# Optimization experiments

Measured on AMD Instinct MI355X. Metric: run time of the kernel, lower is better.

Reference implementation:

```python
import jax, jax.numpy as jnp
from jax import lax
import numpy as np

NUM_HEAD = 4
D_MODEL = 160
HEAD_DIM = D_MODEL // NUM_HEAD  # 40
FEAT_DIM = 64
F_SIZE = (128, 128)
B = 4
LN_EPS = 1e-5
LEAKY_SLOPE = 0.01
DN = ('NCHW', 'OIHW', 'NCHW')


def setup_inputs() -> dict:
    key = jax.random.key(0)
    ks = jax.random.split(key, 10)
    pe_len = (F_SIZE[0] // 2) * (F_SIZE[1] // 2) + 1  # 4097
    s = 0.05
    return {
        'x': jax.random.normal(ks[0], (B, FEAT_DIM, F_SIZE[0], F_SIZE[1]), jnp.float32),
        'conv1_w': jax.random.normal(ks[1], (FEAT_DIM, FEAT_DIM, 2, 2), jnp.float32) * s,
        'conv1_b': jax.random.normal(ks[2], (FEAT_DIM,), jnp.float32) * s,
        'conv2_w': jax.random.normal(ks[3], (D_MODEL, FEAT_DIM, 1, 1), jnp.float32) * s,
        'conv2_b': jax.random.normal(ks[4], (D_MODEL,), jnp.float32) * s,
        'pe': jax.random.uniform(ks[5], (pe_len, 1), jnp.float32),
        'wq': jax.random.normal(ks[6], (D_MODEL, D_MODEL), jnp.float32) * s,
        'wk': jax.random.normal(ks[7], (D_MODEL, D_MODEL), jnp.float32) * s,
        'wv': jax.random.normal(ks[8], (D_MODEL, D_MODEL), jnp.float32) * s,
        'ln_w': jnp.ones((D_MODEL,), jnp.float32),
        'ln_b': jnp.zeros((D_MODEL,), jnp.float32),
    }


def reference(x, conv1_w, conv1_b, conv2_w, conv2_b, pe, wq, wk, wv, ln_w, ln_b):
    b = x.shape[0]
    # patch embed: stride-2 conv -> 1x1 conv -> LeakyReLU
    f = lax.conv_general_dilated(x, conv1_w, (2, 2), 'VALID', dimension_numbers=DN)
    f = f + conv1_b[None, :, None, None]
    f = lax.conv_general_dilated(f, conv2_w, (1, 1), 'VALID', dimension_numbers=DN)
    f = f + conv2_b[None, :, None, None]
    f = jnp.where(f >= 0, f, LEAKY_SLOPE * f)
    _, c, h, w = f.shape  # [b, 160, 64, 64]
    f = f.reshape(b, c, h * w).transpose(0, 2, 1)  # [b, s, d]
    # pad one extra token at end of sequence, add positional encoding [s+1, 1]
    f = jnp.pad(f, ((0, 0), (0, 1), (0, 0))) + pe  # [b, s+1, d]
    s1 = f.shape[1]
    # torch Linear (no bias): y = x @ W.T
    q = (f @ wq.T).reshape(b, s1, NUM_HEAD, HEAD_DIM).transpose(0, 2, 1, 3)
    k = (f @ wk.T).reshape(b, s1, NUM_HEAD, HEAD_DIM).transpose(0, 2, 1, 3)
    v = (f @ wv.T).reshape(b, s1, NUM_HEAD, HEAD_DIM).transpose(0, 2, 1, 3)
    score = jnp.einsum('bhqd,bhkd->bhqk', q, k) / jnp.sqrt(jnp.float32(HEAD_DIM))
    score = jax.nn.softmax(score, axis=-1)
    att = jnp.einsum('bhqk,bhkd->bhqd', score, v)  # [b, h, s+1, hd]
    cat = att.transpose(0, 2, 1, 3).reshape(b, s1, D_MODEL)
    feat = cat[:, :-1, :]  # drop padded token -> [b, s, d]
    # residual LayerNorm: LN(feat) + feat
    mu = jnp.mean(feat, axis=-1, keepdims=True)
    var = jnp.mean(jnp.square(feat - mu), axis=-1, keepdims=True)
    ln = (feat - mu) / jnp.sqrt(var + LN_EPS) * ln_w + ln_b
    feat = ln + feat
    feat = feat.transpose(0, 2, 1).reshape(b, D_MODEL, h, w)  # [b, 160, 64, 64]
    feat = jnp.repeat(jnp.repeat(feat, 2, axis=2), 2, axis=3)
    return feat
```

## Files before the change

kernel.cpp:

```cpp
#include <hip/hip_runtime.h>

typedef _Float16 f16;
typedef _Float16 half2v __attribute__((ext_vector_type(2)));
typedef _Float16 half4v __attribute__((ext_vector_type(4)));
typedef _Float16 half8 __attribute__((ext_vector_type(8)));
typedef float f32x4 __attribute__((ext_vector_type(4)));
typedef unsigned u32x4 __attribute__((ext_vector_type(4)));

#define MFMA16(a, b, c) __builtin_amdgcn_mfma_f32_16x16x32_f16((a), (b), (c), 0, 0, 0)

__device__ __forceinline__ unsigned pk2(float a, float b) {
  return __builtin_bit_cast(unsigned, __builtin_amdgcn_cvt_pkrtz(a, b));
}

__device__ __forceinline__ void plswap_pair(unsigned& a, unsigned& b) {
  asm("s_nop 1\n\t"
      "v_permlane32_swap_b32 %0, %1\n\t"
      "v_permlane16_swap_b32 %0, %1"
      : "+v"(a), "+v"(b));
}


__global__ __launch_bounds__(256) void k_convqkv(
    const float* __restrict__ x, const float* __restrict__ w1, const float* __restrict__ b1,
    const float* __restrict__ w2, const float* __restrict__ b2, const float* __restrict__ pe,
    const float* __restrict__ wq, const float* __restrict__ wk, const float* __restrict__ wv,
    f16* __restrict__ q_h, f16* __restrict__ k_h, f16* __restrict__ vt_h,
    float* __restrict__ kmaxp) {
  __shared__ __attribute__((aligned(16))) char smem[112192];
  f16* fT   = (f16*)smem;
  f16* xh   = (f16*)(smem + 21504);
  f16* wT   = (f16*)(smem + 21504);
  float* red = (float*)(smem + 48384);
  f16* w1h  = (f16*)(smem + 55360);
  f16* c1t  = (f16*)(smem + 55360);
  float* red160 = (float*)(smem + 64576);
  f16* w2h  = (f16*)(smem + 89152);

  int y = blockIdx.x, b = blockIdx.y;
  int t = threadIdx.x, lane = t & 63, wv4 = t >> 6, quad = lane >> 4, col = lane & 15;
  int s0 = y * 64;

  const float* xb = x + (b * 64) * 16384 + (2 * y) * 128;
#pragma unroll
  for (int it = 0; it < 32; ++it) {
    int flat = t + it * 256;
    int pos = flat & 63, r = (flat >> 6) & 1, ci = flat >> 7;
    float2 v = *(const float2*)(xb + ci * 16384 + r * 128 + 2 * pos);
    *(unsigned*)(xh + pos * 264 + ci * 4 + r * 2) = pk2(v.x, v.y);
  }
#pragma unroll
  for (int it = 0; it < 16; ++it) {
    int i4 = t + it * 256;
    int co = i4 >> 6, q4 = (i4 & 63) * 4;
    f32x4 v = *(const f32x4*)(w1 + co * 256 + q4);
    uint2 u = {pk2(v[0], v[1]), pk2(v[2], v[3])};
    *(uint2*)(w1h + co * 264 + q4) = u;
  }
#pragma unroll
  for (int it = 0; it < 10; ++it) {
    int i4 = t + it * 256;
    int c2 = i4 >> 4, q4 = (i4 & 15) * 4;
    f32x4 v = *(const f32x4*)(w2 + c2 * 160 / 160 * 0 + c2 * 64 + q4);
    uint2 u = {pk2(v[0], v[1]), pk2(v[2], v[3])};
    *(uint2*)(w2h + c2 * 72 + q4) = u;
  }
  __syncthreads();

  float b1v[4];
#pragma unroll
  for (int r = 0; r < 4; ++r) b1v[r] = b1[wv4 * 16 + quad * 4 + r];
  f32x4 acc1[4];
#pragma unroll
  for (int nt = 0; nt < 4; ++nt)
#pragma unroll
    for (int r = 0; r < 4; ++r) acc1[nt][r] = b1v[r];
#pragma unroll
  for (int kk = 0; kk < 8; ++kk) {
    half8 a = *(half8*)(w1h + (wv4 * 16 + col) * 264 + kk * 32 + quad * 8);
#pragma unroll
    for (int nt = 0; nt < 4; ++nt) {
      half8 bfr = *(half8*)(xh + (nt * 16 + col) * 264 + kk * 32 + quad * 8);
      acc1[nt] = MFMA16(a, bfr, acc1[nt]);
    }
  }
  __syncthreads();
#pragma unroll
  for (int nt = 0; nt < 4; ++nt) {
    uint2 u = {pk2(acc1[nt][0], acc1[nt][1]), pk2(acc1[nt][2], acc1[nt][3])};
    *(uint2*)(c1t + (nt * 16 + col) * 72 + wv4 * 16 + quad * 4) = u;
  }
  __syncthreads();

  f32x4 acc2[10];
#pragma unroll
  for (int mt = 0; mt < 10; ++mt)
#pragma unroll
    for (int r = 0; r < 4; ++r) acc2[mt][r] = b2[mt * 16 + quad * 4 + r];
  half8 bb0 = *(half8*)(c1t + (wv4 * 16 + col) * 72 + quad * 8);
  half8 bb1 = *(half8*)(c1t + (wv4 * 16 + col) * 72 + 32 + quad * 8);
#pragma unroll
  for (int mt = 0; mt < 10; ++mt) {
    half8 a0 = *(half8*)(w2h + (mt * 16 + col) * 72 + quad * 8);
    half8 a1 = *(half8*)(w2h + (mt * 16 + col) * 72 + 32 + quad * 8);
    acc2[mt] = MFMA16(a0, bb0, acc2[mt]);
    acc2[mt] = MFMA16(a1, bb1, acc2[mt]);
  }
  float pes = pe[s0 + wv4 * 16 + col];
#pragma unroll
  for (int mt = 0; mt < 10; ++mt) {
    float p[4];
#pragma unroll
    for (int r = 0; r < 4; ++r) {
      float v = acc2[mt][r];
      v = (v >= 0.f) ? v : 0.01f * v;
      p[r] = v + pes;
    }
    uint2 u = {pk2(p[0], p[1]), pk2(p[2], p[3])};
    *(uint2*)(fT + (wv4 * 16 + col) * 168 + mt * 16 + quad * 4) = u;
  }
  __syncthreads();

  half8 af[5];
  int rowA = wv4 * 16 + col;
#pragma unroll
  for (int kk = 0; kk < 5; ++kk)
    af[kk] = *(half8*)(fT + rowA * 168 + kk * 32 + quad * 8);

  float ks0[4], ks1[4];
#pragma unroll
  for (int r = 0; r < 4; ++r) { ks0[r] = 0.f; ks1[r] = 0.f; }

  for (int kind = 0; kind < 3; ++kind) {
    const float* wsp = (kind == 0) ? wq : (kind == 1 ? wk : wv);
    for (int hf = 0; hf < 2; ++hf) {
      __syncthreads();
      for (int c = t; c < 1600; c += 256) {
        int row = c / 20, seg = c - row * 20;
        const float* src = wsp + (hf * 80 + row) * 160 + seg * 8;
        f32x4 va = *(const f32x4*)src;
        f32x4 vb = *(const f32x4*)(src + 4);
        uint4 u = {pk2(va[0], va[1]), pk2(va[2], va[3]), pk2(vb[0], vb[1]), pk2(vb[2], vb[3])};
        *(uint4*)(wT + row * 168 + seg * 8) = u;
      }
      __syncthreads();
#pragma unroll
      for (int n0 = 0; n0 < 5; ++n0) {
        f32x4 acc; acc[0] = 0.f; acc[1] = 0.f; acc[2] = 0.f; acc[3] = 0.f;
        int rowB = n0 * 16 + col;
#pragma unroll
        for (int kk = 0; kk < 5; ++kk) {
          half8 bf = *(half8*)(wT + rowB * 168 + kk * 32 + quad * 8);
          acc = MFMA16(af[kk], bf, acc);
        }
        int o = (hf * 5 + n0) * 16 + col;
        int hh = o / 40, d = o - hh * 40;
        int bh = b * 4 + hh;
        if (kind == 1) {
          bool kidx = (n0 * 16 + col) >= 40;
#pragma unroll
          for (int r = 0; r < 4; ++r) {
            float z = acc[r] * acc[r];
            ks0[r] += kidx ? 0.f : z;
            ks1[r] += kidx ? z : 0.f;
          }
        }
#pragma unroll
        for (int r = 0; r < 4; ++r) {
          int s = s0 + wv4 * 16 + quad * 4 + r;
          f16 v = (f16)acc[r];
          if (kind == 0)      q_h[((size_t)bh * 4097 + s) * 40 + d] = v;
          else if (kind == 1) k_h[((size_t)bh * 4160 + s) * 40 + d] = v;
          else                vt_h[((size_t)bh * 40 + d) * 4160 + s] = v;
        }
      }
      if (kind == 1) {
        float m0 = 0.f, m1 = 0.f;
#pragma unroll
        for (int r = 0; r < 4; ++r) {
          float v0 = ks0[r], v1 = ks1[r];
          v0 += __shfl_xor(v0, 1); v0 += __shfl_xor(v0, 2);
          v0 += __shfl_xor(v0, 4); v0 += __shfl_xor(v0, 8);
          v1 += __shfl_xor(v1, 1); v1 += __shfl_xor(v1, 2);
          v1 += __shfl_xor(v1, 4); v1 += __shfl_xor(v1, 8);
          m0 = fmaxf(m0, v0); m1 = fmaxf(m1, v1);
          ks0[r] = 0.f; ks1[r] = 0.f;
        }
        m0 = fmaxf(m0, __shfl_xor(m0, 16)); m0 = fmaxf(m0, __shfl_xor(m0, 32));
        m1 = fmaxf(m1, __shfl_xor(m1, 16)); m1 = fmaxf(m1, __shfl_xor(m1, 32));
        if (lane == 0) { red[wv4 * 4 + hf * 2] = m0; red[wv4 * 4 + hf * 2 + 1] = m1; }
      }
    }
  }
  __syncthreads();
  if (t < 4) {
    float m = fmaxf(fmaxf(red[t], red[4 + t]), fmaxf(red[8 + t], red[12 + t]));
    kmaxp[(b * 4 + t) * 65 + y] = m;
  }

  if (y == 63) {
    float pe4 = pe[4096];
    if (t < 160) {
      int hh = t / 40, d = t - hh * 40, bh = b * 4 + hh;
#pragma unroll
      for (int kind = 0; kind < 3; ++kind) {
        const float* wsp = (kind == 0) ? wq : (kind == 1 ? wk : wv);
        const float* wr = wsp + t * 160;
        float rs = 0.f;
#pragma unroll
        for (int c4 = 0; c4 < 40; ++c4) {
          f32x4 v = *(const f32x4*)(wr + c4 * 4);
          rs += v[0] + v[1] + v[2] + v[3];
        }
        float val = pe4 * rs;
        if (kind == 0)      q_h[((size_t)bh * 4097 + 4096) * 40 + d] = (f16)val;
        else if (kind == 1) { k_h[((size_t)bh * 4160 + 4096) * 40 + d] = (f16)val;
                              red160[t] = val * val; }
        else                vt_h[((size_t)bh * 40 + d) * 4160 + 4096] = (f16)val;
      }
    }
    __syncthreads();
    if (t < 4) {
      float s = 0.f;
#pragma unroll
      for (int j = 0; j < 40; ++j) s += red160[t * 40 + j];
      kmaxp[(b * 4 + t) * 65 + 64] = s;
    }
  }
}

__global__ __launch_bounds__(256, 4) void k_attn(
    const f16* __restrict__ q_h, const f16* __restrict__ k_h,
    const f16* __restrict__ vt_h, const float* __restrict__ kmaxp,
    float* __restrict__ pacc) {
  __shared__ __attribute__((aligned(16))) f16 Ks[2][64 * 40];
  __shared__ __attribute__((aligned(16))) f16 Vs[2][40 * 72];
  __shared__ __attribute__((aligned(16))) f16 Ones[8];
  __shared__ __attribute__((aligned(16))) f16 Zro[8];
  __shared__ __attribute__((aligned(16))) float red4[4];

  int qt = blockIdx.x, bh = blockIdx.y, ks = blockIdx.z;
  int qbase = qt * 128;
  int t = threadIdx.x, lane = t & 63, wv = t >> 6, quad = lane >> 4, col = lane & 15;
  const float c1l = 0.15811388300841898f * 1.4426950408889634f;
  int gbase = ks * 33;
  int nIter = 33 - ks;

  if (t < 8) { Zro[t] = (f16)0; Ones[t] = (f16)1; }
  {
    float vm = (t < 65) ? kmaxp[bh * 65 + t] : 0.f;
#pragma unroll
    for (int d = 1; d < 64; d <<= 1) vm = fmaxf(vm, __shfl_xor(vm, d));
    if (lane == 0) red4[wv] = vm;
  }

  const f16* khb = k_h + ((size_t)bh * 4160 + gbase * 64) * 40;
  const f16* vtb = vt_h + (size_t)bh * 40 * 4160;
  int vrow = t >> 3, vseg = t & 7;
  uint4 rka = *(const uint4*)(khb + t * 8);
  uint4 rkb = {0, 0, 0, 0}, rvb = {0, 0, 0, 0};
  if (t < 64) rkb = *(const uint4*)(khb + (256 + t) * 8);
  uint4 rva = *(const uint4*)(vtb + vrow * 4160 + gbase * 64 + vseg * 8);
  if (t < 64) rvb = *(const uint4*)(vtb + (32 + vrow) * 4160 + gbase * 64 + vseg * 8);

  half8 zero8;
#pragma unroll
  for (int j = 0; j < 8; ++j) zero8[j] = (f16)0;

  half8 bq[2][2];
#pragma unroll
  for (int nt = 0; nt < 2; ++nt) {
    const f16* qr = q_h + ((size_t)bh * 4097 + qbase + wv * 32 + nt * 16 + col) * 40;
    bq[nt][0] = *(const half8*)(qr + quad * 8);
    bq[nt][1] = (quad == 0) ? *(const half8*)(qr + 32) : zero8;
  }
  __syncthreads();

  float mk = fmaxf(fmaxf(red4[0], red4[1]), fmaxf(red4[2], red4[3]));

  float mfl[2];
#pragma unroll
  for (int nt = 0; nt < 2; ++nt) {
    float s = 0.f;
#pragma unroll
    for (int j = 0; j < 8; ++j) {
      float a0 = (float)bq[nt][0][j], a1 = (float)bq[nt][1][j];
      s += a0 * a0 + a1 * a1;
    }
    s += __shfl_xor(s, 16);
    s += __shfl_xor(s, 32);
    mfl[nt] = sqrtf(s * mk) * c1l - 14.0f;
  }

  f32x4 o_[2][3];
#pragma unroll
  for (int a = 0; a < 2; ++a)
#pragma unroll
    for (int b2 = 0; b2 < 3; ++b2)
#pragma unroll
      for (int r = 0; r < 4; ++r) o_[a][b2][r] = 0.f;

  for (int kt = 0; kt < nIter; ++kt) {
    int bsel = kt & 1;
    int g = gbase + kt;
    *(uint4*)(&Ks[bsel][t * 8]) = rka;
    if (t < 64) *(uint4*)(&Ks[bsel][(256 + t) * 8]) = rkb;
    *(uint4*)(&Vs[bsel][vrow * 72 + vseg * 8]) = rva;
    if (t < 64) *(uint4*)(&Vs[bsel][(32 + vrow) * 72 + vseg * 8]) = rvb;
    if (kt + 1 < nIter) {
      const f16* kn = khb + (size_t)(kt + 1) * 2560;
      int k0n = (g + 1) << 6;
      rka = *(const uint4*)(kn + t * 8);
      if (t < 64) rkb = *(const uint4*)(kn + (256 + t) * 8);
      rva = *(const uint4*)(vtb + vrow * 4160 + k0n + vseg * 8);
      if (t < 64) rvb = *(const uint4*)(vtb + (32 + vrow) * 4160 + k0n + vseg * 8);
    }
    __syncthreads();

    bool lastt = (g == 64);
#pragma unroll
    for (int kk2 = 0; kk2 < 2; ++kk2) {
      f32x4 acc[2][2];
#pragma unroll
      for (int hf = 0; hf < 2; ++hf) {
        int mt = kk2 * 2 + hf;
        int row = mt * 16 + col;
        half8 ak0 = *(half8*)(&Ks[bsel][row * 40 + quad * 8]);
        const f16* pa1 = (quad == 0) ? &Ks[bsel][row * 40 + 32] : Zro;
        half8 ak1 = *(half8*)pa1;
#pragma unroll
        for (int nt = 0; nt < 2; ++nt) {
          f32x4 a; a[0] = 0.f; a[1] = 0.f; a[2] = 0.f; a[3] = 0.f;
          a = MFMA16(ak0, bq[nt][0], a);
          a = MFMA16(ak1, bq[nt][1], a);
          acc[hf][nt] = a;
        }
      }
      half8 pa[2];
#pragma unroll
      for (int nt = 0; nt < 2; ++nt) {
        unsigned sr[4];
#pragma unroll
        for (int hf = 0; hf < 2; ++hf) {
          int mt = kk2 * 2 + hf;
          float p[4];
#pragma unroll
          for (int r = 0; r < 4; ++r) {
            p[r] = __builtin_amdgcn_exp2f(fmaf(acc[hf][nt][r], c1l, -mfl[nt]));
            if (lastt && (mt * 16 + quad * 4 + r) != 0) p[r] = 0.f;
          }
          sr[hf * 2]     = pk2(p[0], p[1]);
          sr[hf * 2 + 1] = pk2(p[2], p[3]);
        }
        plswap_pair(sr[0], sr[2]);
        plswap_pair(sr[1], sr[3]);
        u32x4 uu; uu[0] = sr[0]; uu[1] = sr[1]; uu[2] = sr[2]; uu[3] = sr[3];
        pa[nt] = __builtin_bit_cast(half8, uu);
      }
#pragma unroll
      for (int nv = 0; nv < 3; ++nv) {
        int d = nv * 16 + col;
        const f16* vp = (d < 40) ? &Vs[bsel][d * 72 + kk2 * 32 + quad * 8]
                                 : ((d == 40) ? Ones : Zro);
        half8 bv = *(half8*)vp;
        o_[0][nv] = MFMA16(pa[0], bv, o_[0][nv]);
        o_[1][nv] = MFMA16(pa[1], bv, o_[1][nv]);
      }
    }
  }

  float* pb = pacc + (size_t)(ks * 16 + bh) * 4096 * 48;
#pragma unroll
  for (int mtq = 0; mtq < 2; ++mtq)
#pragma unroll
    for (int nv = 0; nv < 3; ++nv)
#pragma unroll
      for (int r = 0; r < 4; ++r) {
        int q = qbase + wv * 32 + mtq * 16 + quad * 4 + r;
        pb[(size_t)q * 48 + nv * 16 + col] = o_[mtq][nv][r];
      }
}

__global__ __launch_bounds__(256) void k_ln_out(
    const float* __restrict__ pacc, const float* __restrict__ lnw,
    const float* __restrict__ lnb, float* __restrict__ out) {
  __shared__ float g[32 * 164];
  __shared__ float linv[32 * 4];
  int y = blockIdx.x, b = blockIdx.y, z = blockIdx.z, t = threadIdx.x;
  const size_t P1 = (size_t)16 * 4096 * 48;
  int w0 = z * 32;
  if (t < 128) {
    int row = t >> 2, h = t & 3;
    size_t i0 = ((size_t)(b * 4 + h) * 4096 + y * 64 + w0 + row) * 48 + 40;
    linv[row * 4 + h] = 1.f / (pacc[i0] + pacc[P1 + i0]);
  }
  __syncthreads();
#pragma unroll
  for (int it = 0; it < 5; ++it) {
    int flat = t + it * 256;
    int row = flat / 40, dq = flat - row * 40;
    int h = dq / 10, d = (dq - h * 10) * 4;
    size_t idx = ((size_t)(b * 4 + h) * 4096 + y * 64 + w0 + row) * 48 + d;
    f32x4 v0 = *(const f32x4*)(pacc + idx);
    f32x4 v1 = *(const f32x4*)(pacc + P1 + idx);
    float li = linv[row * 4 + h];
    f32x4 gv;
#pragma unroll
    for (int j = 0; j < 4; ++j) gv[j] = (v0[j] + v1[j]) * li;
    *(f32x4*)(g + row * 164 + h * 40 + d) = gv;
  }
  __syncthreads();
  int row = t >> 3, part = t & 7;
  float* gr = g + row * 164 + part * 20;
  float s1 = 0.f, s2 = 0.f;
#pragma unroll
  for (int j4 = 0; j4 < 5; ++j4) {
    f32x4 v = *(f32x4*)(gr + j4 * 4);
#pragma unroll
    for (int j = 0; j < 4; ++j) { s1 += v[j]; s2 += v[j] * v[j]; }
  }
  s1 += __shfl_xor(s1, 1); s1 += __shfl_xor(s1, 2); s1 += __shfl_xor(s1, 4);
  s2 += __shfl_xor(s2, 1); s2 += __shfl_xor(s2, 2); s2 += __shfl_xor(s2, 4);
  float mu = s1 * (1.f / 160.f);
  float var = s2 * (1.f / 160.f) - mu * mu;
  float inv = rsqrtf(var + 1e-5f);
  const float* lw = lnw + part * 20;
  const float* lb = lnb + part * 20;
#pragma unroll
  for (int j = 0; j < 20; ++j) {
    float v = gr[j];
    gr[j] = (v - mu) * inv * lw[j] + lb[j] + v;
  }
  __syncthreads();
  int Yo = t >> 7, xp = t & 63, cpar = (t >> 6) & 1;
  int rl = xp >> 1;
  float* ob = out + (2 * y + Yo) * 128 + z * 64 + xp;
  for (int c = cpar; c < 160; c += 2)
    ob[(size_t)(b * 160 + c) * 16384] = g[rl * 164 + c];
}

extern "C" void kernel_launch(void* const* d_in, const int* in_sizes, int n_in,
                              void* d_out, int out_size, void* d_ws, size_t ws_size,
                              hipStream_t stream) {
  const float* x   = (const float*)d_in[0];
  const float* w1  = (const float*)d_in[1];
  const float* b1  = (const float*)d_in[2];
  const float* w2  = (const float*)d_in[3];
  const float* b2  = (const float*)d_in[4];
  const float* pe  = (const float*)d_in[5];
  const float* wq  = (const float*)d_in[6];
  const float* wk  = (const float*)d_in[7];
  const float* wvp = (const float*)d_in[8];
  const float* lnw = (const float*)d_in[9];
  const float* lnb = (const float*)d_in[10];
  float* out = (float*)d_out;

  char* p = (char*)d_ws;
  f16* q_h   = (f16*)p;   p += (size_t)16 * 4097 * 40 * 2;
  f16* k_h   = (f16*)p;   p += (size_t)16 * 4160 * 40 * 2;
  f16* vt_h  = (f16*)p;   p += (size_t)16 * 40 * 4160 * 2;
  float* pacc = (float*)p; p += (size_t)2 * 16 * 4096 * 48 * 4;
  float* kmaxp = (float*)p; p += 16 * 65 * 4;

  k_convqkv<<<dim3(64, 4), 256, 0, stream>>>(x, w1, b1, w2, b2, pe, wq, wk, wvp,
                                             q_h, k_h, vt_h, kmaxp);
  k_attn<<<dim3(32, 16, 2), 256, 0, stream>>>(q_h, k_h, vt_h, kmaxp, pacc);
  k_ln_out<<<dim3(64, 4, 2), 256, 0, stream>>>(pacc, lnw, lnb, out);
}
```

Baseline: 214.3 us.

## Split attention keys three ways, fold softmax scale and max offset into MFMA

```diff
diff --git a/kernel.cpp b/kernel.cpp
--- a/kernel.cpp
+++ b/kernel.cpp
@@ -34,8 +34,11 @@
   float* red = (float*)(smem + 48384);
   f16* w1h  = (f16*)(smem + 55360);
   f16* c1t  = (f16*)(smem + 55360);
+  f16* Lv   = (f16*)(smem + 55360);
   float* red160 = (float*)(smem + 64576);
   f16* w2h  = (f16*)(smem + 89152);
+
+  const float c1l = 0.15811388300841898f * 1.4426950408889634f;
 
   int y = blockIdx.x, b = blockIdx.y;
   int t = threadIdx.x, lane = t & 63, wv4 = t >> 6, quad = lane >> 4, col = lane & 15;
@@ -61,7 +64,7 @@
   for (int it = 0; it < 10; ++it) {
     int i4 = t + it * 256;
     int c2 = i4 >> 4, q4 = (i4 & 15) * 4;
-    f32x4 v = *(const f32x4*)(w2 + c2 * 160 / 160 * 0 + c2 * 64 + q4);
+    f32x4 v = *(const f32x4*)(w2 + c2 * 64 + q4);
     uint2 u = {pk2(v[0], v[1]), pk2(v[2], v[3])};
     *(uint2*)(w2h + c2 * 72 + q4) = u;
   }
@@ -165,13 +168,18 @@
             ks1[r] += kidx ? z : 0.f;
           }
         }
-#pragma unroll
-        for (int r = 0; r < 4; ++r) {
-          int s = s0 + wv4 * 16 + quad * 4 + r;
-          f16 v = (f16)acc[r];
-          if (kind == 0)      q_h[((size_t)bh * 4097 + s) * 40 + d] = v;
-          else if (kind == 1) k_h[((size_t)bh * 4160 + s) * 40 + d] = v;
-          else                vt_h[((size_t)bh * 40 + d) * 4160 + s] = v;
+        if (kind == 2) {
+          half4v hv;
+#pragma unroll
+          for (int r = 0; r < 4; ++r) hv[r] = (f16)acc[r];
+          *(half4v*)(Lv + (n0 * 16 + col) * 72 + wv4 * 16 + quad * 4) = hv;
+        } else {
+#pragma unroll
+          for (int r = 0; r < 4; ++r) {
+            int s = s0 + wv4 * 16 + quad * 4 + r;
+            if (kind == 0)      q_h[((size_t)bh * 4097 + s) * 40 + d] = (f16)(acc[r] * c1l);
+            else                k_h[((size_t)bh * 4160 + s) * 40 + d] = (f16)acc[r];
+          }
         }
       }
       if (kind == 1) {
@@ -190,6 +198,15 @@
         m1 = fmaxf(m1, __shfl_xor(m1, 16)); m1 = fmaxf(m1, __shfl_xor(m1, 32));
         if (lane == 0) { red[wv4 * 4 + hf * 2] = m0; red[wv4 * 4 + hf * 2 + 1] = m1; }
       }
+      if (kind == 2) {
+        __syncthreads();
+        for (int c = t; c < 640; c += 256) {
+          int row = c >> 3, seg = c & 7;
+          int o = hf * 80 + row, hh = o / 40, d = o - hh * 40;
+          *(uint4*)(vt_h + ((size_t)(b * 4 + hh) * 40 + d) * 4160 + s0 + seg * 8) =
+              *(const uint4*)(Lv + row * 72 + seg * 8);
+        }
+      }
     }
   }
   __syncthreads();
@@ -213,7 +230,7 @@
           rs += v[0] + v[1] + v[2] + v[3];
         }
         float val = pe4 * rs;
-        if (kind == 0)      q_h[((size_t)bh * 4097 + 4096) * 40 + d] = (f16)val;
+        if (kind == 0)      q_h[((size_t)bh * 4097 + 4096) * 40 + d] = (f16)(val * c1l);
         else if (kind == 1) { k_h[((size_t)bh * 4160 + 4096) * 40 + d] = (f16)val;
                               red160[t] = val * val; }
         else                vt_h[((size_t)bh * 40 + d) * 4160 + 4096] = (f16)val;
@@ -229,7 +246,7 @@
   }
 }
 
-__global__ __launch_bounds__(256, 4) void k_attn(
+__global__ __launch_bounds__(256, 6) void k_attn(
     const f16* __restrict__ q_h, const f16* __restrict__ k_h,
     const f16* __restrict__ vt_h, const float* __restrict__ kmaxp,
     float* __restrict__ pacc) {
@@ -242,9 +259,8 @@
   int qt = blockIdx.x, bh = blockIdx.y, ks = blockIdx.z;
   int qbase = qt * 128;
   int t = threadIdx.x, lane = t & 63, wv = t >> 6, quad = lane >> 4, col = lane & 15;
-  const float c1l = 0.15811388300841898f * 1.4426950408889634f;
-  int gbase = ks * 33;
-  int nIter = 33 - ks;
+  int gbase = ks * 22;
+  int nIter = (ks == 2) ? 21 : 22;
 
   if (t < 8) { Zro[t] = (f16)0; Ones[t] = (f16)1; }
   {
@@ -267,29 +283,36 @@
 #pragma unroll
   for (int j = 0; j < 8; ++j) zero8[j] = (f16)0;
 
-  half8 bq[2][2];
+  half8 bq[2][2], q32[2];
 #pragma unroll
   for (int nt = 0; nt < 2; ++nt) {
     const f16* qr = q_h + ((size_t)bh * 4097 + qbase + wv * 32 + nt * 16 + col) * 40;
     bq[nt][0] = *(const half8*)(qr + quad * 8);
-    bq[nt][1] = (quad == 0) ? *(const half8*)(qr + 32) : zero8;
+    q32[nt] = *(const half8*)(qr + 32);
   }
   __syncthreads();
 
   float mk = fmaxf(fmaxf(red4[0], red4[1]), fmaxf(red4[2], red4[3]));
 
-  float mfl[2];
 #pragma unroll
   for (int nt = 0; nt < 2; ++nt) {
     float s = 0.f;
 #pragma unroll
     for (int j = 0; j < 8; ++j) {
-      float a0 = (float)bq[nt][0][j], a1 = (float)bq[nt][1][j];
-      s += a0 * a0 + a1 * a1;
+      float a0 = (float)bq[nt][0][j];
+      s += a0 * a0;
     }
     s += __shfl_xor(s, 16);
     s += __shfl_xor(s, 32);
-    mfl[nt] = sqrtf(s * mk) * c1l - 14.0f;
+#pragma unroll
+    for (int j = 0; j < 8; ++j) {
+      float a1 = (float)q32[nt][j];
+      s += a1 * a1;
+    }
+    float mfl = sqrtf(s * mk) - 14.0f;
+    half8 e = zero8;
+    e[0] = (f16)(-mfl);
+    bq[nt][1] = (quad == 0) ? q32[nt] : ((quad == 1) ? e : zero8);
   }
 
   f32x4 o_[2][3];
@@ -326,7 +349,8 @@
         int mt = kk2 * 2 + hf;
         int row = mt * 16 + col;
         half8 ak0 = *(half8*)(&Ks[bsel][row * 40 + quad * 8]);
-        const f16* pa1 = (quad == 0) ? &Ks[bsel][row * 40 + 32] : Zro;
+        const f16* pa1 = (quad == 0) ? &Ks[bsel][row * 40 + 32]
+                                     : ((quad == 1) ? Ones : Zro);
         half8 ak1 = *(half8*)pa1;
 #pragma unroll
         for (int nt = 0; nt < 2; ++nt) {
@@ -339,19 +363,24 @@
       half8 pa[2];
 #pragma unroll
       for (int nt = 0; nt < 2; ++nt) {
+        float p0[4], p1[4];
+#pragma unroll
+        for (int r = 0; r < 4; ++r) {
+          p0[r] = __builtin_amdgcn_exp2f(acc[0][nt][r]);
+          p1[r] = __builtin_amdgcn_exp2f(acc[1][nt][r]);
+        }
+        if (__builtin_expect(lastt, 0)) {
+#pragma unroll
+          for (int r = 0; r < 4; ++r) {
+            p0[r] = ((kk2 * 2) * 16 + quad * 4 + r) == 0 ? p0[r] : 0.f;
+            p1[r] = 0.f;
+          }
+        }
         unsigned sr[4];
-#pragma unroll
-        for (int hf = 0; hf < 2; ++hf) {
-          int mt = kk2 * 2 + hf;
-          float p[4];
-#pragma unroll
-          for (int r = 0; r < 4; ++r) {
-            p[r] = __builtin_amdgcn_exp2f(fmaf(acc[hf][nt][r], c1l, -mfl[nt]));
-            if (lastt && (mt * 16 + quad * 4 + r) != 0) p[r] = 0.f;
-          }
-          sr[hf * 2]     = pk2(p[0], p[1]);
-          sr[hf * 2 + 1] = pk2(p[2], p[3]);
-        }
+        sr[0] = pk2(p0[0], p0[1]);
+        sr[1] = pk2(p0[2], p0[3]);
+        sr[2] = pk2(p1[0], p1[1]);
+        sr[3] = pk2(p1[2], p1[3]);
         plswap_pair(sr[0], sr[2]);
         plswap_pair(sr[1], sr[3]);
         u32x4 uu; uu[0] = sr[0]; uu[1] = sr[1]; uu[2] = sr[2]; uu[3] = sr[3];
@@ -392,7 +421,7 @@
   if (t < 128) {
     int row = t >> 2, h = t & 3;
     size_t i0 = ((size_t)(b * 4 + h) * 4096 + y * 64 + w0 + row) * 48 + 40;
-    linv[row * 4 + h] = 1.f / (pacc[i0] + pacc[P1 + i0]);
+    linv[row * 4 + h] = 1.f / (pacc[i0] + pacc[P1 + i0] + pacc[2 * P1 + i0]);
   }
   __syncthreads();
 #pragma unroll
@@ -403,10 +432,11 @@
     size_t idx = ((size_t)(b * 4 + h) * 4096 + y * 64 + w0 + row) * 48 + d;
     f32x4 v0 = *(const f32x4*)(pacc + idx);
     f32x4 v1 = *(const f32x4*)(pacc + P1 + idx);
+    f32x4 v2 = *(const f32x4*)(pacc + 2 * P1 + idx);
     float li = linv[row * 4 + h];
     f32x4 gv;
 #pragma unroll
-    for (int j = 0; j < 4; ++j) gv[j] = (v0[j] + v1[j]) * li;
+    for (int j = 0; j < 4; ++j) gv[j] = (v0[j] + v1[j] + v2[j]) * li;
     *(f32x4*)(g + row * 164 + h * 40 + d) = gv;
   }
   __syncthreads();
@@ -459,11 +489,11 @@
   f16* q_h   = (f16*)p;   p += (size_t)16 * 4097 * 40 * 2;
   f16* k_h   = (f16*)p;   p += (size_t)16 * 4160 * 40 * 2;
   f16* vt_h  = (f16*)p;   p += (size_t)16 * 40 * 4160 * 2;
-  float* pacc = (float*)p; p += (size_t)2 * 16 * 4096 * 48 * 4;
+  float* pacc = (float*)p; p += (size_t)3 * 16 * 4096 * 48 * 4;
   float* kmaxp = (float*)p; p += 16 * 65 * 4;
 
   k_convqkv<<<dim3(64, 4), 256, 0, stream>>>(x, w1, b1, w2, b2, pe, wq, wk, wvp,
                                              q_h, k_h, vt_h, kmaxp);
-  k_attn<<<dim3(32, 16, 2), 256, 0, stream>>>(q_h, k_h, vt_h, kmaxp, pacc);
+  k_attn<<<dim3(32, 16, 3), 256, 0, stream>>>(q_h, k_h, vt_h, kmaxp, pacc);
   k_ln_out<<<dim3(64, 4, 2), 256, 0, stream>>>(pacc, lnw, lnb, out);
 }
```

New measurement: 245.9 us. 14.8% more time.
